# Optimization experiments

Measured on AMD Instinct MI355X. Metric: run time of the kernel, lower is better.

The kernel has to match this reference:

```python
import jax, jax.numpy as jnp
import numpy as np

L, H, NH, NKV, HD, I, V, B, S = 18, 640, 4, 1, 256, 2048, 32768, 1, 1024
WINDOW = 512
EPS = 1e-6
THETA_G = 1000000.0
THETA_L = 10000.0


def _rms(x, w):
    # Gemma RMSNorm: x / rms(x) * (1 + w)
    var = jnp.mean(jnp.square(x), axis=-1, keepdims=True)
    return x * jax.lax.rsqrt(var + EPS) * (1.0 + w)


def _rope_tables(theta):
    inv = 1.0 / (theta ** (jnp.arange(0, HD, 2, dtype=jnp.float32) / HD))
    f = jnp.arange(S, dtype=jnp.float32)[:, None] * inv[None, :]
    emb = jnp.concatenate([f, f], axis=-1)  # [S, HD]
    return jnp.cos(emb), jnp.sin(emb)


def _rope(x, cos, sin):
    # x: [B, S, n, HD]
    x1, x2 = jnp.split(x, 2, axis=-1)
    rot = jnp.concatenate([-x2, x1], axis=-1)
    return x * cos[None, :, None, :] + rot * sin[None, :, None, :]


def setup_inputs() -> dict:
    key = jax.random.key(0)
    ks = jax.random.split(key, 16)
    r = lambda k, sh: jax.random.normal(k, sh, jnp.float32) * 0.02
    return {
        'input_ids': jax.random.randint(ks[0], (B, S), 0, V, jnp.int32),
        'is_full': jnp.array([(i + 1) % 6 == 0 for i in range(L)]),
        'embed': r(ks[1], (V, H)),
        'wq': r(ks[2], (L, H, NH * HD)),
        'wk': r(ks[3], (L, H, NKV * HD)),
        'wv': r(ks[4], (L, H, NKV * HD)),
        'wo': r(ks[5], (L, NH * HD, H)),
        'qn': jnp.zeros((L, HD)), 'kn': jnp.zeros((L, HD)),
        'ln1': jnp.zeros((L, H)), 'ln2': jnp.zeros((L, H)),
        'ln3': jnp.zeros((L, H)), 'ln4': jnp.zeros((L, H)),
        'wg': r(ks[6], (L, H, I)), 'wu': r(ks[7], (L, H, I)),
        'wd': r(ks[8], (L, I, H)),
        'norm_w': jnp.zeros((H,)),
    }


def _forward(embed, wq, wk, wv, wo, qn, kn, ln1, ln2, ln3, ln4, wg, wu, wd,
             norm_w, input_ids, is_full):
    cos_g, sin_g = _rope_tables(THETA_G)
    cos_l, sin_l = _rope_tables(THETA_L)
    pos = jnp.arange(S)
    causal = pos[:, None] >= pos[None, :]
    sliding = causal & ((pos[:, None] - pos[None, :]) < WINDOW)
    scale = HD ** -0.5
    grp = NH // NKV

    h = embed[input_ids] * jnp.asarray(H ** 0.5, embed.dtype)  # [B,S,H]

    def body(h, xs):
        (wq_, wk_, wv_, wo_, qn_, kn_, l1, l2, l3, l4, wg_, wu_, wd_, full) = xs
        cos = jnp.where(full, cos_g, cos_l)
        sin = jnp.where(full, sin_g, sin_l)
        mask = jnp.where(full, causal, sliding)
        x = _rms(h, l1)
        q = (x @ wq_).reshape(B, S, NH, HD)
        k = (x @ wk_).reshape(B, S, NKV, HD)
        v = (x @ wv_).reshape(B, S, NKV, HD)
        q = _rope(_rms(q, qn_), cos, sin)
        k = _rope(_rms(k, kn_), cos, sin)
        qg = q.reshape(B, S, NKV, grp, HD)
        scores = jnp.einsum('bqngd,bsnd->bngqs', qg, k) * scale
        scores = jnp.where(mask[None, None, None], scores, -1e30)
        attn = jax.nn.softmax(scores, axis=-1)
        o = jnp.einsum('bngqs,bsnd->bqngd', attn, v).reshape(B, S, NH * HD)
        h = h + _rms(o @ wo_, l2)               # post_attention_layernorm then residual
        x = _rms(h, l3)                          # pre_feedforward_layernorm
        mlp = (jax.nn.gelu(x @ wg_, approximate=True) * (x @ wu_)) @ wd_  # GeGLU
        h = h + _rms(mlp, l4)                    # post_feedforward_layernorm then residual
        return h, None

    h, _ = jax.lax.scan(body, h, (wq, wk, wv, wo, qn, kn, ln1, ln2, ln3, ln4, wg, wu, wd, is_full))
    h = _rms(h, norm_w)
    # lm_head tied to embed_tokens; final_logit_softcapping = 0.0 (disabled)
    return jnp.einsum('bsh,vh->bsv', h, embed)


def reference(input_ids, is_full, embed, wq, wk, wv, wo, qn, kn,
              ln1, ln2, ln3, ln4, wg, wu, wd, norm_w):
    return _forward(embed, wq, wk, wv, wo, qn, kn, ln1, ln2, ln3, ln4,
                    wg, wu, wd, norm_w, input_ids, is_full)
```

## Files before the change

kernel.cpp:

```cpp
#include <hip/hip_runtime.h>


typedef unsigned short u16;
typedef __attribute__((ext_vector_type(4))) float f32x4;
typedef __attribute__((ext_vector_type(8))) short bf16x8;

#define DEV static __device__ __forceinline__

DEV u16 f2bf(float f) {
  union { float f; unsigned u; } x; x.f = f;
  unsigned r = x.u + 0x7fffu + ((x.u >> 16) & 1u);
  return (u16)(r >> 16);
}

#define GLOAD16(gp, lp) __builtin_amdgcn_global_load_lds( \
    (const __attribute__((address_space(1))) void*)(gp), \
    (__attribute__((address_space(3))) void*)(lp), 16, 0, 0)

DEV float blockSum(float v, float* red) {
#pragma unroll
  for (int o = 32; o; o >>= 1) v += __shfl_down(v, o);
  int lane = threadIdx.x & 63, wid = threadIdx.x >> 6;
  if (lane == 0) red[wid] = v;
  __syncthreads();
  float s = red[0] + red[1] + red[2] + red[3];
  __syncthreads();
  return s;
}

DEV float blockMax(float v, float* red) {
#pragma unroll
  for (int o = 32; o; o >>= 1) v = fmaxf(v, __shfl_down(v, o));
  int lane = threadIdx.x & 63, wid = threadIdx.x >> 6;
  if (lane == 0) red[wid] = v;
  __syncthreads();
  float s = fmaxf(fmaxf(red[0], red[1]), fmaxf(red[2], red[3]));
  __syncthreads();
  return s;
}

DEV void cstore(float* C, size_t i, float v) { C[i] = v; }
DEV void cstore(u16* C, size_t i, float v) { C[i] = f2bf(v); }

template <typename CT, int GEGLU>
__global__ __launch_bounds__(256) void gemm_nt(
    const u16* __restrict__ A, int lda, long sA,
    const u16* __restrict__ B, int ldb, long sB,
    CT* __restrict__ C, int ldc, long sC,
    int K, float alpha, int kmode, int nshift, int ksplit) {
  __shared__ __align__(16) u16 As[2 * 128 * 64];
  __shared__ __align__(16) u16 Bs[2 * 128 * 64];
  const int m0 = blockIdx.y * 128;
  int n0;
  if (nshift == -1) n0 = blockIdx.x * 128;
  else if (nshift == -2) { n0 = blockIdx.x * 128; if (n0 > m0) return; }
  else { n0 = m0 - nshift + blockIdx.x * 128; if (n0 < 0) return; }
  int klo = 0, khi = K;
  if (kmode == 1) { klo = m0 - 512; if (klo < 0) klo = 0; khi = m0 + 128; if (khi > K) khi = K; }
  else if (kmode == 2) { khi = m0 + 128; if (khi > K) khi = K; }
  else if (kmode == 3) { int kl = K / ksplit; klo = blockIdx.z * kl; khi = klo + kl; }
  A += (long)blockIdx.z * sA;
  B += (long)blockIdx.z * sB;

  const int t = threadIdx.x;
  const int l = t & 63, w = t >> 6;
  const int wr = w >> 1, wc = w & 1;
  const int lr = l & 15, lk = l >> 4;
  const int axr = lr & 7;
  const int srow = t >> 3;
  const int scolx = ((t & 7) ^ (srow & 7)) << 3;
  const u16* Ag = A + (size_t)(m0 + srow) * lda + scolx;
  const u16* Bg = B + (size_t)(n0 + srow) * ldb + scolx;
  const int nsteps = (khi - klo) >> 6;

  auto stage = [&](int db, int k0) {
    const u16* a = Ag + k0;
    const u16* b = Bg + k0;
    u16* al = As + db * 8192 + w * 512;
    u16* bl = Bs + db * 8192 + w * 512;
#pragma unroll
    for (int p = 0; p < 4; ++p) {
      GLOAD16(a + (size_t)(32 * p) * lda, al + p * 2048);
      GLOAD16(b + (size_t)(32 * p) * ldb, bl + p * 2048);
    }
  };

  stage(0, klo);
  f32x4 acc[4][4] = {};

  for (int s = 0; s < nsteps; ++s) {
    __syncthreads();
    const int db = s & 1;
    if (s + 1 < nsteps) stage(db ^ 1, klo + (s + 1) * 64);
    const u16* Ab = As + db * 8192;
    const u16* Bb = Bs + db * 8192;
    bf16x8 af[2][4], bfr[2][4];
#pragma unroll
    for (int kk = 0; kk < 2; ++kk)
#pragma unroll
      for (int i = 0; i < 4; ++i) {
        af[kk][i]  = *(const bf16x8*)&Ab[(wr * 64 + i * 16 + lr) * 64 + (((kk * 4 + lk) ^ axr) << 3)];
        bfr[kk][i] = *(const bf16x8*)&Bb[(wc * 64 + i * 16 + lr) * 64 + (((kk * 4 + lk) ^ axr) << 3)];
      }
#pragma unroll
    for (int kk = 0; kk < 2; ++kk)
#pragma unroll
      for (int mi = 0; mi < 4; ++mi)
#pragma unroll
        for (int ni = 0; ni < 4; ++ni)
          acc[mi][ni] = __builtin_amdgcn_mfma_f32_16x16x32_bf16(af[kk][mi], bfr[kk][ni], acc[mi][ni], 0, 0, 0);
  }

  C += (long)blockIdx.z * sC;
  if (GEGLU) {
#pragma unroll
    for (int mi = 0; mi < 4; ++mi) {
      int row = m0 + wr * 64 + mi * 16 + lk * 4;
#pragma unroll
      for (int np = 0; np < 2; ++np) {
        int col = (n0 + wc * 64) / 2 + np * 16 + lr;
#pragma unroll
        for (int j = 0; j < 4; ++j) {
          float g = acc[mi][2 * np][j], u = acc[mi][2 * np + 1][j];
          float z = 0.7978845608028654f * (g + 0.044715f * g * g * g);
          float th = 2.0f / (1.0f + __expf(-2.0f * z)) - 1.0f;
          cstore(C, (size_t)(row + j) * ldc + col, 0.5f * g * (1.0f + th) * u);
        }
      }
    }
  } else {
#pragma unroll
    for (int mi = 0; mi < 4; ++mi) {
      int row = m0 + wr * 64 + mi * 16 + lk * 4;
#pragma unroll
      for (int ni = 0; ni < 4; ++ni) {
        int col = n0 + wc * 64 + ni * 16 + lr;
#pragma unroll
        for (int j = 0; j < 4; ++j)
          cstore(C, (size_t)(row + j) * ldc + col, acc[mi][ni][j] * alpha);
      }
    }
  }
}

__global__ void conv_bf16_kernel(const float* __restrict__ in, u16* __restrict__ out, long n4) {
  for (long i = (long)blockIdx.x * blockDim.x + threadIdx.x; i < n4; i += (long)gridDim.x * blockDim.x) {
    float4 v = ((const float4*)in)[i];
    ushort4 o4 = { f2bf(v.x), f2bf(v.y), f2bf(v.z), f2bf(v.w) };
    ((ushort4*)out)[i] = o4;
  }
}

__global__ void gather_kernel(const int* __restrict__ ids, const float* __restrict__ embed,
                              float* __restrict__ h) {
  int s = blockIdx.x;
  const float* src = embed + (size_t)ids[s] * 640;
  float scale = sqrtf(640.0f);
  for (int c = threadIdx.x; c < 640; c += blockDim.x)
    h[(size_t)s * 640 + c] = src[c] * scale;
}

__global__ void rms_to_bf16(const float* __restrict__ in, const float* __restrict__ w,
                            u16* __restrict__ out, int n) {
  __shared__ float red[8];
  int row = blockIdx.x;
  const float* x = in + (size_t)row * n;
  float ss = 0.0f;
  for (int c = threadIdx.x; c < n; c += blockDim.x) { float v = x[c]; ss += v * v; }
  ss = blockSum(ss, red);
  float sc = rsqrtf(ss / (float)n + 1e-6f);
  for (int c = threadIdx.x; c < n; c += blockDim.x)
    out[(size_t)row * n + c] = f2bf(x[c] * sc * (1.0f + w[c]));
}

__global__ void fused_add_norm(float* __restrict__ h, const float* __restrict__ t1,
                               int nsl, const float* __restrict__ wa,
                               const float* __restrict__ wn, u16* __restrict__ xout) {
  __shared__ float red[8];
  const int row = blockIdx.x, t = threadIdx.x;
  float ts[3], hv[3];
  float ss = 0.0f;
#pragma unroll
  for (int i = 0; i < 3; ++i) {
    int c = t + i * 256;
    float v = 0.0f;
    if (c < 640) {
      v = t1[(size_t)row * 640 + c];
      for (int z = 1; z < nsl; ++z) v += t1[(size_t)z * 655360 + (size_t)row * 640 + c];
    }
    ts[i] = v; ss += v * v;
  }
  ss = blockSum(ss, red);
  const float s1 = rsqrtf(ss * (1.0f / 640.0f) + 1e-6f);
  float ss2 = 0.0f;
#pragma unroll
  for (int i = 0; i < 3; ++i) {
    int c = t + i * 256;
    float v = 0.0f;
    if (c < 640) v = h[(size_t)row * 640 + c] + ts[i] * s1 * (1.0f + wa[c]);
    hv[i] = v; ss2 += v * v;
  }
  ss2 = blockSum(ss2, red);
  const float s2 = rsqrtf(ss2 * (1.0f / 640.0f) + 1e-6f);
#pragma unroll
  for (int i = 0; i < 3; ++i) {
    int c = t + i * 256;
    if (c < 640) {
      h[(size_t)row * 640 + c] = hv[i];
      xout[(size_t)row * 640 + c] = f2bf(hv[i] * s2 * (1.0f + wn[c]));
    }
  }
}

__global__ void rope_tables_kernel(float* cg, float* sg, float* cl, float* sl) {
  int s = blockIdx.x, t = threadIdx.x;
  float e = -(float)t * (1.0f / 128.0f);
  float ag = (float)s * expf(e * logf(1000000.0f));
  float al = (float)s * expf(e * logf(10000.0f));
  cg[s * 128 + t] = cosf(ag); sg[s * 128 + t] = sinf(ag);
  cl[s * 128 + t] = cosf(al); sl[s * 128 + t] = sinf(al);
}

__global__ void rope_fused(const float* __restrict__ qkvf, const float* __restrict__ qn,
                           const float* __restrict__ kn, u16* __restrict__ qb,
                           u16* __restrict__ kb, u16* __restrict__ vt,
                           const float* __restrict__ ct, const float* __restrict__ st) {
  __shared__ float red[8];
  __shared__ float sh[256];
  const int s = blockIdx.x, hh = blockIdx.y, t = threadIdx.x;
  if (hh == 5) {
    vt[(size_t)t * 1024 + s] = f2bf(qkvf[(size_t)s * 1536 + 1280 + t]);
    return;
  }
  const float* src = qkvf + (size_t)s * 1536 + hh * 256;
  const float* nw = (hh == 4) ? kn : qn;
  float x = src[t];
  float ss = blockSum(x * x, red);
  float n = x * rsqrtf(ss * (1.0f / 256.0f) + 1e-6f) * (1.0f + nw[t]);
  sh[t] = n;
  __syncthreads();
  float cosv = ct[s * 128 + (t & 127)];
  float sinv = st[s * 128 + (t & 127)];
  float partner = (t < 128) ? -sh[t + 128] : sh[t - 128];
  u16 r = f2bf(n * cosv + partner * sinv);
  if (hh == 4) kb[(size_t)s * 256 + t] = r;
  else qb[((size_t)hh * 1024 + s) * 256 + t] = r;
}

__global__ void softmax_kernel(const float* __restrict__ sc, u16* __restrict__ P, int mode) {
  __shared__ float red[8];
  const int i = blockIdx.x, hh = blockIdx.y, t = threadIdx.x;
  const float* row = sc + ((size_t)hh * 1024 + i) * 1024;
  u16* prow = P + ((size_t)hh * 1024 + i) * 1024;
  const int m0 = i & ~127;
  int lo = 0, wlo = 0;
  if (mode) {
    lo = i - 511; if (lo < 0) lo = 0;
    wlo = m0 - 512; if (wlo < 0) wlo = 0;
  }
  const int whi = m0 + 127;
  float m = -1e30f;
  for (int j = lo + t; j <= i; j += 256) m = fmaxf(m, row[j]);
  m = blockMax(m, red);
  float sum = 0.0f;
  for (int j = lo + t; j <= i; j += 256) sum += __expf(row[j] - m);
  sum = blockSum(sum, red);
  float inv = 1.0f / sum;
  for (int j = wlo + t; j <= whi; j += 256) {
    float v = (j >= lo && j <= i) ? __expf(row[j] - m) * inv : 0.0f;
    prow[j] = f2bf(v);
  }
}

__global__ void transpose7_kernel(
    const float* s0, const float* s1, const float* s2, const float* s3,
    const float* s4, const float* s5, const float* s6,
    u16* d0, u16* d1, u16* d2, u16* d3, u16* d45, u16* d6) {
  __shared__ float tile[64][65];
  int b = blockIdx.x;
  const float* src; u16* dst; int K, N, idx, ilv = 0;
  if (b < 160)       { src = s0; dst = d0;  K = 640;  N = 1024; idx = b; }
  else if (b < 200)  { src = s1; dst = d1;  K = 640;  N = 256;  idx = b - 160; }
  else if (b < 240)  { src = s2; dst = d2;  K = 640;  N = 256;  idx = b - 200; }
  else if (b < 400)  { src = s3; dst = d3;  K = 1024; N = 640;  idx = b - 240; }
  else if (b < 720)  { src = s4; dst = d45; K = 640;  N = 2048; idx = b - 400;  ilv = 1; }
  else if (b < 1040) { src = s5; dst = d45; K = 640;  N = 2048; idx = b - 720;  ilv = 2; }
  else               { src = s6; dst = d6;  K = 2048; N = 640;  idx = b - 1040; }
  int tn = N >> 6;
  int kt = idx / tn, nt = idx % tn;
  int t = threadIdx.x;
  int lr = t >> 4, lc = (t & 15) * 4;
#pragma unroll
  for (int i = 0; i < 4; ++i) {
    float4 v = *(const float4*)&src[(size_t)(kt * 64 + lr + i * 16) * N + nt * 64 + lc];
    tile[lr + i * 16][lc] = v.x; tile[lr + i * 16][lc + 1] = v.y;
    tile[lr + i * 16][lc + 2] = v.z; tile[lr + i * 16][lc + 3] = v.w;
  }
  __syncthreads();
  int wn = t >> 3, wk8 = (t & 7) * 8;
#pragma unroll
  for (int i = 0; i < 2; ++i) {
    int gcol = nt * 64 + wn + i * 32;
    int drow = ilv ? ((gcol >> 4) * 32 + ((ilv == 2) ? 16 : 0) + (gcol & 15)) : gcol;
    u16 tmp[8];
#pragma unroll
    for (int j = 0; j < 8; ++j) tmp[j] = f2bf(tile[wk8 + j][wn + i * 32]);
    *(int4*)&dst[(size_t)drow * K + kt * 64 + wk8] = *(int4*)tmp;
  }
}

extern "C" void kernel_launch(void* const* d_in, const int* in_sizes, int n_in,
                              void* d_out, int out_size, void* d_ws, size_t ws_size,
                              hipStream_t stream) {
  (void)in_sizes; (void)n_in; (void)out_size; (void)ws_size;
  const int*   ids   = (const int*)d_in[0];
  const float* embed = (const float*)d_in[2];
  const float* wq    = (const float*)d_in[3];
  const float* wk    = (const float*)d_in[4];
  const float* wv    = (const float*)d_in[5];
  const float* wo    = (const float*)d_in[6];
  const float* qn    = (const float*)d_in[7];
  const float* kn    = (const float*)d_in[8];
  const float* ln1   = (const float*)d_in[9];
  const float* ln2   = (const float*)d_in[10];
  const float* ln3   = (const float*)d_in[11];
  const float* ln4   = (const float*)d_in[12];
  const float* wg    = (const float*)d_in[13];
  const float* wu    = (const float*)d_in[14];
  const float* wd    = (const float*)d_in[15];
  const float* nw    = (const float*)d_in[16];
  float* out = (float*)d_out;

  const int S = 1024, H = 640, NH = 4, HD = 256, I = 2048, V = 32768;

  unsigned char* p = (unsigned char*)d_ws;
  auto alloc = [&](size_t b) { void* r = (void*)p; p += (b + 255) & ~(size_t)255; return r; };
  u16*   wqkvT = (u16*)alloc((size_t)1536 * 640 * 2);
  u16*   woT   = (u16*)alloc((size_t)640 * 1024 * 2);
  u16*   wguT  = (u16*)alloc((size_t)4096 * 640 * 2);
  u16*   wdT   = (u16*)alloc((size_t)640 * 2048 * 2);
  u16*   embT  = (u16*)alloc((size_t)V * H * 2);
  float* h     = (float*)alloc((size_t)S * H * 4);
  u16*   x     = (u16*)alloc((size_t)S * H * 2);
  float* qkvf  = (float*)alloc((size_t)S * 1536 * 4);
  u16*   qb    = (u16*)alloc((size_t)NH * S * HD * 2);
  u16*   kb    = (u16*)alloc((size_t)S * HD * 2);
  u16*   vt    = (u16*)alloc((size_t)HD * S * 2);
  float* scp   = (float*)alloc((size_t)NH * S * S * 4);
  u16*   P     = (u16*)alloc((size_t)NH * S * S * 2);
  u16*   o     = (u16*)alloc((size_t)S * NH * HD * 2);
  float* t1    = (float*)alloc((size_t)4 * S * H * 4);
  u16*   mg    = (u16*)alloc((size_t)S * I * 2);
  u16*   hn    = (u16*)alloc((size_t)S * H * 2);
  float* cg    = (float*)alloc((size_t)S * 128 * 4);
  float* sg    = (float*)alloc((size_t)S * 128 * 4);
  float* cl    = (float*)alloc((size_t)S * 128 * 4);
  float* sl2   = (float*)alloc((size_t)S * 128 * 4);

  rope_tables_kernel<<<S, 128, 0, stream>>>(cg, sg, cl, sl2);
  conv_bf16_kernel<<<2048, 256, 0, stream>>>(embed, embT, (long)V * H / 4);
  gather_kernel<<<S, 256, 0, stream>>>(ids, embed, h);
  rms_to_bf16<<<S, 256, 0, stream>>>(h, ln1, x, H);

  for (int l = 0; l < 18; ++l) {
    bool full = ((l + 1) % 6) == 0;

    transpose7_kernel<<<1360, 256, 0, stream>>>(
        wq + (size_t)l * H * 1024, wk + (size_t)l * H * 256, wv + (size_t)l * H * 256,
        wo + (size_t)l * 1024 * H, wg + (size_t)l * H * I, wu + (size_t)l * H * I,
        wd + (size_t)l * I * H,
        wqkvT, wqkvT + (size_t)1024 * 640, wqkvT + (size_t)1280 * 640, woT, wguT, wdT);

    gemm_nt<float, 0><<<dim3(12, 8, 1), 256, 0, stream>>>(
        x, H, 0, wqkvT, H, 0, qkvf, 1536, 0, H, 1.0f, 0, -1, 1);
    rope_fused<<<dim3(S, 6), 256, 0, stream>>>(qkvf, qn + l * HD, kn + l * HD, qb, kb, vt,
                                               full ? cg : cl, full ? sg : sl2);
    if (full)
      gemm_nt<float, 0><<<dim3(8, 8, NH), 256, 0, stream>>>(
          qb, HD, (long)S * HD, kb, HD, 0, scp, S, (long)S * S, HD, 0.0625f, 0, -2, 1);
    else
      gemm_nt<float, 0><<<dim3(5, 8, NH), 256, 0, stream>>>(
          qb, HD, (long)S * HD, kb, HD, 0, scp, S, (long)S * S, HD, 0.0625f, 0, 512, 1);
    softmax_kernel<<<dim3(S, NH), 256, 0, stream>>>(scp, P, full ? 0 : 1);
    gemm_nt<u16, 0><<<dim3(2, 8, NH), 256, 0, stream>>>(
        P, S, (long)S * S, vt, S, 0, o, NH * HD, HD, S, 1.0f, full ? 2 : 1, -1, 1);
    gemm_nt<float, 0><<<dim3(5, 8, 2), 256, 0, stream>>>(
        o, NH * HD, 0, woT, NH * HD, 0, t1, H, (long)S * H, NH * HD, 1.0f, 3, -1, 2);
    fused_add_norm<<<S, 256, 0, stream>>>(h, t1, 2, ln2 + l * H, ln3 + l * H, x);

    gemm_nt<u16, 1><<<dim3(32, 8, 1), 256, 0, stream>>>(
        x, H, 0, wguT, H, 0, mg, I, 0, H, 1.0f, 0, -1, 1);
    gemm_nt<float, 0><<<dim3(5, 8, 4), 256, 0, stream>>>(
        mg, I, 0, wdT, I, 0, t1, H, (long)S * H, I, 1.0f, 3, -1, 4);
    fused_add_norm<<<S, 256, 0, stream>>>(h, t1, 4, ln4 + l * H,
                                          (l == 17) ? nw : ln1 + (l + 1) * H,
                                          (l == 17) ? hn : x);
  }

  gemm_nt<float, 0><<<dim3(V / 128, 8, 1), 256, 0, stream>>>(
      hn, H, 0, embT, H, 0, out, V, 0, H, 1.0f, 0, -1, 1);
}
```

Baseline: 2.080 ms.

## Fuse softmax into PV GEMM, batch weight transposes, use 64-row GEMM tiles

Removes the standalone softmax kernel and the bf16 probability buffer. A new pv_fused kernel computes row max and sum from the fp32 scores, then builds the bf16 probabilities on the fly while multiplying by V. The weight transposes for all 18 layers now run in one batched launch when the workspace is large enough, instead of once per layer. The GEMM template gains a BM parameter so the smaller GEMMs use 64-row tiles and launch more blocks. The cost is that the fused kernel reads the fp32 scores twice and recomputes exp per element, and batching needs a larger workspace.

```diff
diff --git a/kernel.cpp b/kernel.cpp
--- a/kernel.cpp
+++ b/kernel.cpp
@@ -28,36 +28,25 @@
   return s;
 }
 
-DEV float blockMax(float v, float* red) {
-#pragma unroll
-  for (int o = 32; o; o >>= 1) v = fmaxf(v, __shfl_down(v, o));
-  int lane = threadIdx.x & 63, wid = threadIdx.x >> 6;
-  if (lane == 0) red[wid] = v;
-  __syncthreads();
-  float s = fmaxf(fmaxf(red[0], red[1]), fmaxf(red[2], red[3]));
-  __syncthreads();
-  return s;
-}
-
 DEV void cstore(float* C, size_t i, float v) { C[i] = v; }
 DEV void cstore(u16* C, size_t i, float v) { C[i] = f2bf(v); }
 
-template <typename CT, int GEGLU>
+template <typename CT, int GEGLU, int BM>
 __global__ __launch_bounds__(256) void gemm_nt(
     const u16* __restrict__ A, int lda, long sA,
     const u16* __restrict__ B, int ldb, long sB,
     CT* __restrict__ C, int ldc, long sC,
-    int K, float alpha, int kmode, int nshift, int ksplit) {
-  __shared__ __align__(16) u16 As[2 * 128 * 64];
+    int K, float alpha, int kmode, int nshift, int ksplit, int nmax) {
+  constexpr int MI = BM / 32;
+  __shared__ __align__(16) u16 As[2 * BM * 64];
   __shared__ __align__(16) u16 Bs[2 * 128 * 64];
-  const int m0 = blockIdx.y * 128;
+  const int m0 = blockIdx.y * BM;
   int n0;
   if (nshift == -1) n0 = blockIdx.x * 128;
   else if (nshift == -2) { n0 = blockIdx.x * 128; if (n0 > m0) return; }
-  else { n0 = m0 - nshift + blockIdx.x * 128; if (n0 < 0) return; }
+  else { n0 = ((m0 - nshift) & ~127) + blockIdx.x * 128; if (n0 < 0) return; }
   int klo = 0, khi = K;
-  if (kmode == 1) { klo = m0 - 512; if (klo < 0) klo = 0; khi = m0 + 128; if (khi > K) khi = K; }
-  else if (kmode == 2) { khi = m0 + 128; if (khi > K) khi = K; }
+  if (kmode == 2) { khi = m0 + BM; if (khi > K) khi = K; }
   else if (kmode == 3) { int kl = K / ksplit; klo = blockIdx.z * kl; khi = klo + kl; }
   A += (long)blockIdx.z * sA;
   B += (long)blockIdx.z * sB;
@@ -74,38 +63,39 @@
   const int nsteps = (khi - klo) >> 6;
 
   auto stage = [&](int db, int k0) {
-    const u16* a = Ag + k0;
-    const u16* b = Bg + k0;
-    u16* al = As + db * 8192 + w * 512;
+    u16* al = As + db * (BM * 64) + w * 512;
     u16* bl = Bs + db * 8192 + w * 512;
 #pragma unroll
-    for (int p = 0; p < 4; ++p) {
-      GLOAD16(a + (size_t)(32 * p) * lda, al + p * 2048);
-      GLOAD16(b + (size_t)(32 * p) * ldb, bl + p * 2048);
-    }
+    for (int p = 0; p < BM / 32; ++p)
+      GLOAD16(Ag + k0 + (size_t)(32 * p) * lda, al + p * 2048);
+#pragma unroll
+    for (int p = 0; p < 4; ++p)
+      GLOAD16(Bg + k0 + (size_t)(32 * p) * ldb, bl + p * 2048);
   };
 
   stage(0, klo);
-  f32x4 acc[4][4] = {};
+  f32x4 acc[MI][4] = {};
 
   for (int s = 0; s < nsteps; ++s) {
     __syncthreads();
     const int db = s & 1;
     if (s + 1 < nsteps) stage(db ^ 1, klo + (s + 1) * 64);
-    const u16* Ab = As + db * 8192;
+    const u16* Ab = As + db * (BM * 64);
     const u16* Bb = Bs + db * 8192;
-    bf16x8 af[2][4], bfr[2][4];
+    bf16x8 af[2][MI], bfr[2][4];
+#pragma unroll
+    for (int kk = 0; kk < 2; ++kk) {
+#pragma unroll
+      for (int i = 0; i < MI; ++i)
+        af[kk][i] = *(const bf16x8*)&Ab[(wr * (BM / 2) + i * 16 + lr) * 64 + (((kk * 4 + lk) ^ axr) << 3)];
+#pragma unroll
+      for (int i = 0; i < 4; ++i)
+        bfr[kk][i] = *(const bf16x8*)&Bb[(wc * 64 + i * 16 + lr) * 64 + (((kk * 4 + lk) ^ axr) << 3)];
+    }
 #pragma unroll
     for (int kk = 0; kk < 2; ++kk)
 #pragma unroll
-      for (int i = 0; i < 4; ++i) {
-        af[kk][i]  = *(const bf16x8*)&Ab[(wr * 64 + i * 16 + lr) * 64 + (((kk * 4 + lk) ^ axr) << 3)];
-        bfr[kk][i] = *(const bf16x8*)&Bb[(wc * 64 + i * 16 + lr) * 64 + (((kk * 4 + lk) ^ axr) << 3)];
-      }
-#pragma unroll
-    for (int kk = 0; kk < 2; ++kk)
-#pragma unroll
-      for (int mi = 0; mi < 4; ++mi)
+      for (int mi = 0; mi < MI; ++mi)
 #pragma unroll
         for (int ni = 0; ni < 4; ++ni)
           acc[mi][ni] = __builtin_amdgcn_mfma_f32_16x16x32_bf16(af[kk][mi], bfr[kk][ni], acc[mi][ni], 0, 0, 0);
@@ -114,8 +104,8 @@
   C += (long)blockIdx.z * sC;
   if (GEGLU) {
 #pragma unroll
-    for (int mi = 0; mi < 4; ++mi) {
-      int row = m0 + wr * 64 + mi * 16 + lk * 4;
+    for (int mi = 0; mi < MI; ++mi) {
+      int row = m0 + wr * (BM / 2) + mi * 16 + lk * 4;
 #pragma unroll
       for (int np = 0; np < 2; ++np) {
         int col = (n0 + wc * 64) / 2 + np * 16 + lr;
@@ -130,15 +120,125 @@
     }
   } else {
 #pragma unroll
-    for (int mi = 0; mi < 4; ++mi) {
-      int row = m0 + wr * 64 + mi * 16 + lk * 4;
+    for (int mi = 0; mi < MI; ++mi) {
+      int row = m0 + wr * (BM / 2) + mi * 16 + lk * 4;
 #pragma unroll
       for (int ni = 0; ni < 4; ++ni) {
         int col = n0 + wc * 64 + ni * 16 + lr;
-#pragma unroll
-        for (int j = 0; j < 4; ++j)
-          cstore(C, (size_t)(row + j) * ldc + col, acc[mi][ni][j] * alpha);
+        if (col < nmax)
+#pragma unroll
+          for (int j = 0; j < 4; ++j)
+            cstore(C, (size_t)(row + j) * ldc + col, acc[mi][ni][j] * alpha);
       }
+    }
+  }
+}
+
+__global__ __launch_bounds__(256) void pv_fused(
+    const float* __restrict__ scp, const u16* __restrict__ vt,
+    u16* __restrict__ o, int isfull) {
+  __shared__ __align__(16) u16 Bs[2 * 128 * 64];
+  __shared__ float mrow[64], invl[64];
+  const int z = blockIdx.z, m0 = blockIdx.y * 64, n0 = blockIdx.x * 128;
+  const float* S_ = scp + (size_t)z * 1024 * 1024;
+  const int t = threadIdx.x;
+
+  {
+    int r = t >> 2, q = t & 3;
+    int row = m0 + r;
+    int lo = isfull ? 0 : (row - 511 > 0 ? row - 511 : 0);
+    const float* rp = S_ + (size_t)row * 1024;
+    float mx = -1e30f;
+    for (int j = lo + q; j <= row; j += 4) mx = fmaxf(mx, rp[j]);
+    mx = fmaxf(mx, __shfl_xor(mx, 1));
+    mx = fmaxf(mx, __shfl_xor(mx, 2));
+    float sum = 0.0f;
+    for (int j = lo + q; j <= row; j += 4) sum += __expf(rp[j] - mx);
+    sum += __shfl_xor(sum, 1);
+    sum += __shfl_xor(sum, 2);
+    if (q == 0) { mrow[r] = mx; invl[r] = 1.0f / sum; }
+  }
+  __syncthreads();
+
+  const int l = t & 63, w = t >> 6;
+  const int wr = w >> 1, wc = w & 1;
+  const int lr = l & 15, lk = l >> 4;
+  const int axr = lr & 7;
+  const int srow = t >> 3;
+  const int scolx = ((t & 7) ^ (srow & 7)) << 3;
+  const u16* Bg = vt + (size_t)(n0 + srow) * 1024 + scolx;
+  int klo = isfull ? 0 : (m0 - 512 > 0 ? m0 - 512 : 0);
+  int khi = m0 + 64;
+  const int nsteps = (khi - klo) >> 6;
+
+  auto stageB = [&](int db, int k0) {
+    u16* bl = Bs + db * 8192 + w * 512;
+#pragma unroll
+    for (int p = 0; p < 4; ++p)
+      GLOAD16(Bg + k0 + (size_t)(32 * p) * 1024, bl + p * 2048);
+  };
+  stageB(0, klo);
+
+  int rowi[2]; float ms[2], ls[2];
+#pragma unroll
+  for (int i = 0; i < 2; ++i) {
+    rowi[i] = wr * 32 + i * 16 + lr;
+    ms[i] = mrow[rowi[i]];
+    ls[i] = invl[rowi[i]];
+  }
+
+  f32x4 acc[2][4] = {};
+  for (int s = 0; s < nsteps; ++s) {
+    __syncthreads();
+    const int db = s & 1;
+    if (s + 1 < nsteps) stageB(db ^ 1, klo + (s + 1) * 64);
+    const int k0 = klo + s * 64;
+    bf16x8 af[2][2];
+#pragma unroll
+    for (int kk = 0; kk < 2; ++kk)
+#pragma unroll
+      for (int i = 0; i < 2; ++i) {
+        int row = m0 + rowi[i];
+        int kb = k0 + kk * 32 + lk * 8;
+        const float* ap = S_ + (size_t)row * 1024 + kb;
+        float4 v0 = *(const float4*)ap;
+        float4 v1 = *(const float4*)(ap + 4);
+        float vv[8] = {v0.x, v0.y, v0.z, v0.w, v1.x, v1.y, v1.z, v1.w};
+        int lo = isfull ? 0 : row - 511;
+        u16 tmp[8];
+#pragma unroll
+        for (int e = 0; e < 8; ++e) {
+          int k = kb + e;
+          float pv = __expf(vv[e] - ms[i]) * ls[i];
+          tmp[e] = f2bf((k >= lo && k <= row) ? pv : 0.0f);
+        }
+        af[kk][i] = *(bf16x8*)tmp;
+      }
+    const u16* Bb = Bs + db * 8192;
+    bf16x8 bfr[2][4];
+#pragma unroll
+    for (int kk = 0; kk < 2; ++kk)
+#pragma unroll
+      for (int i = 0; i < 4; ++i)
+        bfr[kk][i] = *(const bf16x8*)&Bb[(wc * 64 + i * 16 + lr) * 64 + (((kk * 4 + lk) ^ axr) << 3)];
+#pragma unroll
+    for (int kk = 0; kk < 2; ++kk)
+#pragma unroll
+      for (int mi = 0; mi < 2; ++mi)
+#pragma unroll
+        for (int ni = 0; ni < 4; ++ni)
+          acc[mi][ni] = __builtin_amdgcn_mfma_f32_16x16x32_bf16(af[kk][mi], bfr[kk][ni], acc[mi][ni], 0, 0, 0);
+  }
+
+#pragma unroll
+  for (int mi = 0; mi < 2; ++mi) {
+    int row = m0 + wr * 32 + mi * 16 + lk * 4;
+#pragma unroll
+    for (int ni = 0; ni < 4; ++ni) {
+      int col = z * 256 + n0 + wc * 64 + ni * 16 + lr;
+#pragma unroll
+      for (int j = 0; j < 4; ++j)
+        o[(size_t)(row + j) * 1024 + col] = f2bf(acc[mi][ni][j]);
     }
   }
 }
@@ -247,45 +347,21 @@
   else qb[((size_t)hh * 1024 + s) * 256 + t] = r;
 }
 
-__global__ void softmax_kernel(const float* __restrict__ sc, u16* __restrict__ P, int mode) {
-  __shared__ float red[8];
-  const int i = blockIdx.x, hh = blockIdx.y, t = threadIdx.x;
-  const float* row = sc + ((size_t)hh * 1024 + i) * 1024;
-  u16* prow = P + ((size_t)hh * 1024 + i) * 1024;
-  const int m0 = i & ~127;
-  int lo = 0, wlo = 0;
-  if (mode) {
-    lo = i - 511; if (lo < 0) lo = 0;
-    wlo = m0 - 512; if (wlo < 0) wlo = 0;
-  }
-  const int whi = m0 + 127;
-  float m = -1e30f;
-  for (int j = lo + t; j <= i; j += 256) m = fmaxf(m, row[j]);
-  m = blockMax(m, red);
-  float sum = 0.0f;
-  for (int j = lo + t; j <= i; j += 256) sum += __expf(row[j] - m);
-  sum = blockSum(sum, red);
-  float inv = 1.0f / sum;
-  for (int j = wlo + t; j <= whi; j += 256) {
-    float v = (j >= lo && j <= i) ? __expf(row[j] - m) * inv : 0.0f;
-    prow[j] = f2bf(v);
-  }
-}
-
 __global__ void transpose7_kernel(
     const float* s0, const float* s1, const float* s2, const float* s3,
     const float* s4, const float* s5, const float* s6,
     u16* d0, u16* d1, u16* d2, u16* d3, u16* d45, u16* d6) {
   __shared__ float tile[64][65];
+  const int ly = blockIdx.y;
   int b = blockIdx.x;
   const float* src; u16* dst; int K, N, idx, ilv = 0;
-  if (b < 160)       { src = s0; dst = d0;  K = 640;  N = 1024; idx = b; }
-  else if (b < 200)  { src = s1; dst = d1;  K = 640;  N = 256;  idx = b - 160; }
-  else if (b < 240)  { src = s2; dst = d2;  K = 640;  N = 256;  idx = b - 200; }
-  else if (b < 400)  { src = s3; dst = d3;  K = 1024; N = 640;  idx = b - 240; }
-  else if (b < 720)  { src = s4; dst = d45; K = 640;  N = 2048; idx = b - 400;  ilv = 1; }
-  else if (b < 1040) { src = s5; dst = d45; K = 640;  N = 2048; idx = b - 720;  ilv = 2; }
-  else               { src = s6; dst = d6;  K = 2048; N = 640;  idx = b - 1040; }
+  if (b < 160)       { src = s0 + (size_t)ly * 655360;  dst = d0 + (size_t)ly * 983040;  K = 640;  N = 1024; idx = b; }
+  else if (b < 200)  { src = s1 + (size_t)ly * 163840;  dst = d1 + (size_t)ly * 983040;  K = 640;  N = 256;  idx = b - 160; }
+  else if (b < 240)  { src = s2 + (size_t)ly * 163840;  dst = d2 + (size_t)ly * 983040;  K = 640;  N = 256;  idx = b - 200; }
+  else if (b < 400)  { src = s3 + (size_t)ly * 655360;  dst = d3 + (size_t)ly * 655360;  K = 1024; N = 640;  idx = b - 240; }
+  else if (b < 720)  { src = s4 + (size_t)ly * 1310720; dst = d45 + (size_t)ly * 2621440; K = 640; N = 2048; idx = b - 400;  ilv = 1; }
+  else if (b < 1040) { src = s5 + (size_t)ly * 1310720; dst = d45 + (size_t)ly * 2621440; K = 640; N = 2048; idx = b - 720;  ilv = 2; }
+  else               { src = s6 + (size_t)ly * 1310720; dst = d6 + (size_t)ly * 1310720; K = 2048; N = 640; idx = b - 1040; }
   int tn = N >> 6;
   int kt = idx / tn, nt = idx % tn;
   int t = threadIdx.x;
@@ -312,7 +388,7 @@
 extern "C" void kernel_launch(void* const* d_in, const int* in_sizes, int n_in,
                               void* d_out, int out_size, void* d_ws, size_t ws_size,
                               hipStream_t stream) {
-  (void)in_sizes; (void)n_in; (void)out_size; (void)ws_size;
+  (void)in_sizes; (void)n_in; (void)out_size;
   const int*   ids   = (const int*)d_in[0];
   const float* embed = (const float*)d_in[2];
   const float* wq    = (const float*)d_in[3];
@@ -332,13 +408,17 @@
   float* out = (float*)d_out;
 
   const int S = 1024, H = 640, NH = 4, HD = 256, I = 2048, V = 32768;
+  const int BIG = 1 << 30;
+
+  const bool batched = ws_size >= (size_t)310 * 1024 * 1024;
+  const int NL = batched ? 18 : 1;
 
   unsigned char* p = (unsigned char*)d_ws;
   auto alloc = [&](size_t b) { void* r = (void*)p; p += (b + 255) & ~(size_t)255; return r; };
-  u16*   wqkvT = (u16*)alloc((size_t)1536 * 640 * 2);
-  u16*   woT   = (u16*)alloc((size_t)640 * 1024 * 2);
-  u16*   wguT  = (u16*)alloc((size_t)4096 * 640 * 2);
-  u16*   wdT   = (u16*)alloc((size_t)640 * 2048 * 2);
+  u16*   wqkvT = (u16*)alloc((size_t)NL * 1536 * 640 * 2);
+  u16*   woT   = (u16*)alloc((size_t)NL * 640 * 1024 * 2);
+  u16*   wguT  = (u16*)alloc((size_t)NL * 4096 * 640 * 2);
+  u16*   wdT   = (u16*)alloc((size_t)NL * 640 * 2048 * 2);
   u16*   embT  = (u16*)alloc((size_t)V * H * 2);
   float* h     = (float*)alloc((size_t)S * H * 4);
   u16*   x     = (u16*)alloc((size_t)S * H * 2);
@@ -347,7 +427,6 @@
   u16*   kb    = (u16*)alloc((size_t)S * HD * 2);
   u16*   vt    = (u16*)alloc((size_t)HD * S * 2);
   float* scp   = (float*)alloc((size_t)NH * S * S * 4);
-  u16*   P     = (u16*)alloc((size_t)NH * S * S * 2);
   u16*   o     = (u16*)alloc((size_t)S * NH * HD * 2);
   float* t1    = (float*)alloc((size_t)4 * S * H * 4);
   u16*   mg    = (u16*)alloc((size_t)S * I * 2);
@@ -362,41 +441,50 @@
   gather_kernel<<<S, 256, 0, stream>>>(ids, embed, h);
   rms_to_bf16<<<S, 256, 0, stream>>>(h, ln1, x, H);
 
+  if (batched)
+    transpose7_kernel<<<dim3(1360, 18), 256, 0, stream>>>(
+        wq, wk, wv, wo, wg, wu, wd,
+        wqkvT, wqkvT + (size_t)1024 * 640, wqkvT + (size_t)1280 * 640, woT, wguT, wdT);
+
   for (int l = 0; l < 18; ++l) {
     bool full = ((l + 1) % 6) == 0;
-
-    transpose7_kernel<<<1360, 256, 0, stream>>>(
-        wq + (size_t)l * H * 1024, wk + (size_t)l * H * 256, wv + (size_t)l * H * 256,
-        wo + (size_t)l * 1024 * H, wg + (size_t)l * H * I, wu + (size_t)l * H * I,
-        wd + (size_t)l * I * H,
-        wqkvT, wqkvT + (size_t)1024 * 640, wqkvT + (size_t)1280 * 640, woT, wguT, wdT);
-
-    gemm_nt<float, 0><<<dim3(12, 8, 1), 256, 0, stream>>>(
-        x, H, 0, wqkvT, H, 0, qkvf, 1536, 0, H, 1.0f, 0, -1, 1);
+    size_t lw = batched ? (size_t)l : 0;
+    u16* wqkvTl = wqkvT + lw * 1536 * 640;
+    u16* woTl   = woT   + lw * 640 * 1024;
+    u16* wguTl  = wguT  + lw * 4096 * 640;
+    u16* wdTl   = wdT   + lw * 640 * 2048;
+
+    if (!batched)
+      transpose7_kernel<<<dim3(1360, 1), 256, 0, stream>>>(
+          wq + (size_t)l * H * 1024, wk + (size_t)l * H * 256, wv + (size_t)l * H * 256,
+          wo + (size_t)l * 1024 * H, wg + (size_t)l * H * I, wu + (size_t)l * H * I,
+          wd + (size_t)l * I * H,
+          wqkvTl, wqkvTl + (size_t)1024 * 640, wqkvTl + (size_t)1280 * 640, woTl, wguTl, wdTl);
+
+    gemm_nt<float, 0, 64><<<dim3(12, 16, 1), 256, 0, stream>>>(
+        x, H, 0, wqkvTl, H, 0, qkvf, 1536, 0, H, 1.0f, 0, -1, 1, BIG);
     rope_fused<<<dim3(S, 6), 256, 0, stream>>>(qkvf, qn + l * HD, kn + l * HD, qb, kb, vt,
                                                full ? cg : cl, full ? sg : sl2);
     if (full)
-      gemm_nt<float, 0><<<dim3(8, 8, NH), 256, 0, stream>>>(
-          qb, HD, (long)S * HD, kb, HD, 0, scp, S, (long)S * S, HD, 0.0625f, 0, -2, 1);
+      gemm_nt<float, 0, 64><<<dim3(8, 16, NH), 256, 0, stream>>>(
+          qb, HD, (long)S * HD, kb, HD, 0, scp, S, (long)S * S, HD, 0.0625f, 0, -2, 1, BIG);
     else
-      gemm_nt<float, 0><<<dim3(5, 8, NH), 256, 0, stream>>>(
-          qb, HD, (long)S * HD, kb, HD, 0, scp, S, (long)S * S, HD, 0.0625f, 0, 512, 1);
-    softmax_kernel<<<dim3(S, NH), 256, 0, stream>>>(scp, P, full ? 0 : 1);
-    gemm_nt<u16, 0><<<dim3(2, 8, NH), 256, 0, stream>>>(
-        P, S, (long)S * S, vt, S, 0, o, NH * HD, HD, S, 1.0f, full ? 2 : 1, -1, 1);
-    gemm_nt<float, 0><<<dim3(5, 8, 2), 256, 0, stream>>>(
-        o, NH * HD, 0, woT, NH * HD, 0, t1, H, (long)S * H, NH * HD, 1.0f, 3, -1, 2);
+      gemm_nt<float, 0, 64><<<dim3(5, 16, NH), 256, 0, stream>>>(
+          qb, HD, (long)S * HD, kb, HD, 0, scp, S, (long)S * S, HD, 0.0625f, 0, 512, 1, S);
+    pv_fused<<<dim3(2, 16, NH), 256, 0, stream>>>(scp, vt, o, full ? 1 : 0);
+    gemm_nt<float, 0, 64><<<dim3(5, 16, 2), 256, 0, stream>>>(
+        o, NH * HD, 0, woTl, NH * HD, 0, t1, H, (long)S * H, NH * HD, 1.0f, 3, -1, 2, BIG);
     fused_add_norm<<<S, 256, 0, stream>>>(h, t1, 2, ln2 + l * H, ln3 + l * H, x);
 
-    gemm_nt<u16, 1><<<dim3(32, 8, 1), 256, 0, stream>>>(
-        x, H, 0, wguT, H, 0, mg, I, 0, H, 1.0f, 0, -1, 1);
-    gemm_nt<float, 0><<<dim3(5, 8, 4), 256, 0, stream>>>(
-        mg, I, 0, wdT, I, 0, t1, H, (long)S * H, I, 1.0f, 3, -1, 4);
+    gemm_nt<u16, 1, 128><<<dim3(32, 8, 1), 256, 0, stream>>>(
+        x, H, 0, wguTl, H, 0, mg, I, 0, H, 1.0f, 0, -1, 1, BIG);
+    gemm_nt<float, 0, 64><<<dim3(5, 16, 4), 256, 0, stream>>>(
+        mg, I, 0, wdTl, I, 0, t1, H, (long)S * H, I, 1.0f, 3, -1, 4, BIG);
     fused_add_norm<<<S, 256, 0, stream>>>(h, t1, 4, ln4 + l * H,
                                           (l == 17) ? nw : ln1 + (l + 1) * H,
                                           (l == 17) ? hn : x);
   }
 
-  gemm_nt<float, 0><<<dim3(V / 128, 8, 1), 256, 0, stream>>>(
-      hn, H, 0, embT, H, 0, out, V, 0, H, 1.0f, 0, -1, 1);
-}
+  gemm_nt<float, 0, 128><<<dim3(V / 128, 8, 1), 256, 0, stream>>>(
+      hn, H, 0, embT, H, 0, out, V, 0, H, 1.0f, 0, -1, 1, BIG);
+}
```

After: 2.646 ms. +27.2%, slower.
